# Performance work log

Hardware: AMD Instinct MI355X
Metric: run time of the kernel (lower is better)

The kernel has to match this reference:

```python
import jax, jax.numpy as jnp
import numpy as np
import math

B, S, DIM = 2, 2048, 4096
NH, NKV, HD = 32, 8, 128
N_REP = NH // NKV


def _rope_freqs(seq_len, head_dim, theta=10000.0):
    inv = 1.0 / (theta ** (np.arange(0, head_dim, 2)[: head_dim // 2].astype(np.float32) / head_dim))
    ang = np.outer(np.arange(seq_len, dtype=np.float32), inv)  # [S, HD/2]
    return jnp.asarray(np.cos(ang)), jnp.asarray(np.sin(ang))


def apply_rope(x, cos, sin):
    # x: [B, S, H, HD]; pairs along last dim act as complex numbers
    xr = x.reshape(*x.shape[:-1], HD // 2, 2)
    real, imag = xr[..., 0], xr[..., 1]
    c = cos[None, :, None, :]
    s = sin[None, :, None, :]
    out_r = real * c - imag * s
    out_i = real * s + imag * c
    return jnp.stack([out_r, out_i], axis=-1).reshape(x.shape)


def setup_inputs() -> dict:
    key = jax.random.key(0)
    ks = jax.random.split(key, 6)
    scale = 1.0 / math.sqrt(DIM)
    cos, sin = _rope_freqs(S, HD)
    return {
        "x": jax.random.normal(ks[0], (B, S, DIM), jnp.float32),
        "wq": jax.random.normal(ks[1], (DIM, NH * HD), jnp.float32) * scale,
        "wk": jax.random.normal(ks[2], (DIM, NKV * HD), jnp.float32) * scale,
        "wv": jax.random.normal(ks[3], (DIM, NKV * HD), jnp.float32) * scale,
        "wo": jax.random.normal(ks[4], (NH * HD, DIM), jnp.float32) * scale,
        "cache_k": jnp.zeros((B, S, NKV, HD), jnp.float32),
        "cache_v": jnp.zeros((B, S, NKV, HD), jnp.float32),
        "freqs_cos": cos,
        "freqs_sin": sin,
        "start_pos": 0,
    }


def reference(x, wq, wk, wv, wo, cache_k, cache_v, freqs_cos, freqs_sin, start_pos):
    b, s, _ = x.shape
    xq = (x @ wq).reshape(b, s, NH, HD)
    xk = (x @ wk).reshape(b, s, NKV, HD)
    xv = (x @ wv).reshape(b, s, NKV, HD)

    xq = apply_rope(xq, freqs_cos, freqs_sin)
    xk = apply_rope(xk, freqs_cos, freqs_sin)

    # KV-cache write
    cache_k = jax.lax.dynamic_update_slice(cache_k, xk, (0, start_pos, 0, 0))
    cache_v = jax.lax.dynamic_update_slice(cache_v, xv, (0, start_pos, 0, 0))
    keys = cache_k[:b, : start_pos + s]    # [B, T, NKV, HD]
    values = cache_v[:b, : start_pos + s]

    # GQA repeat_kv: each kv head repeated n_rep times consecutively
    keys = jnp.repeat(keys, N_REP, axis=2)      # [B, T, NH, HD]
    values = jnp.repeat(values, N_REP, axis=2)

    scores = jnp.einsum("bqhd,bkhd->bhqk", xq, keys) / math.sqrt(HD)
    probs = jax.nn.softmax(scores.astype(jnp.float32), axis=-1).astype(xq.dtype)
    out = jnp.einsum("bhqk,bkhd->bqhd", probs, values)
    out = out.reshape(b, s, NH * HD)
    return out @ wo
```

## Files before the change

### kernel.cpp

```cpp
#include <hip/hip_runtime.h>

#define S_LEN 2048
#define DIMC  4096
#define NH    32
#define NKV   8
#define HD    128
#define BATCH 2
#define M_TOT (BATCH*S_LEN)
#define N_QKV (DIMC + 2*NKV*HD)

typedef unsigned short u16;
typedef unsigned int   uint32;
typedef __attribute__((ext_vector_type(8))) short  short8;
typedef __attribute__((ext_vector_type(4))) float  f32x4;
typedef __attribute__((ext_vector_type(4))) float  fvec4;
typedef __attribute__((ext_vector_type(4))) unsigned short u16x4;

__device__ __forceinline__ u16 f2bf(float f) {
    union { float f; unsigned u; } v; v.f = f;
    unsigned r = v.u + 0x7FFFu + ((v.u >> 16) & 1u);
    return (u16)(r >> 16);
}
__device__ __forceinline__ float bf2f(u16 h) {
    union { unsigned u; float f; } v; v.u = ((unsigned)h) << 16;
    return v.f;
}

__device__ __forceinline__ void gload_lds16(const void* g, void* l) {
    __builtin_amdgcn_global_load_lds(
        (const __attribute__((address_space(1))) void*)g,
        (__attribute__((address_space(3))) void*)l, 16, 0, 0);
}

__global__ void cvt_f32_bf16(const float* __restrict__ in, u16* __restrict__ out, int n4) {
    int i = blockIdx.x * 256 + threadIdx.x;
    if (i >= n4) return;
    fvec4 v = ((const fvec4*)in)[i];
    u16x4 o;
    o[0] = f2bf(v[0]); o[1] = f2bf(v[1]); o[2] = f2bf(v[2]); o[3] = f2bf(v[3]);
    ((u16x4*)out)[i] = o;
}

__global__ void transpose_cvt(const float* __restrict__ in, u16* __restrict__ out,
                              int K, int N) {
    __shared__ float tile[32][33];
    int k0 = blockIdx.y * 32, n0 = blockIdx.x * 32;
    int t = threadIdx.x;
    int r = t >> 3, c4 = (t & 7) * 4;
    fvec4 v = *(const fvec4*)&in[(size_t)(k0 + r) * N + n0 + c4];
    tile[r][c4 + 0] = v[0]; tile[r][c4 + 1] = v[1];
    tile[r][c4 + 2] = v[2]; tile[r][c4 + 3] = v[3];
    __syncthreads();
    u16x4 o;
    o[0] = f2bf(tile[c4 + 0][r]); o[1] = f2bf(tile[c4 + 1][r]);
    o[2] = f2bf(tile[c4 + 2][r]); o[3] = f2bf(tile[c4 + 3][r]);
    *(u16x4*)&out[(size_t)(n0 + r) * K + k0 + c4] = o;
}

#define FEN asm volatile("" ::: "memory")
#define BAR1 do { FEN; __builtin_amdgcn_s_barrier(); \
                  asm volatile("s_waitcnt lgkmcnt(0)" ::: "memory"); } while(0)
#define BAR2 do { FEN; __builtin_amdgcn_s_barrier(); FEN; } while(0)

#define LDA(bufc, mh) do { _Pragma("unroll") for (int q_=0;q_<4;++q_) \
    _Pragma("unroll") for (int ks_=0;ks_<2;++ks_) \
    a[q_][ks_] = *(const short8*)(lds + ((bufc)*65536 + ((mh)*4+q_)*2048 + ks_*1024) + aB); } while(0)

#define LDB(bs, bufc, nh) do { _Pragma("unroll") for (int p_=0;p_<2;++p_) \
    _Pragma("unroll") for (int ks_=0;ks_<2;++ks_) \
    bs[p_][ks_] = *(const short8*)(lds + ((bufc)*65536 + ((nh)*2+p_)*2048 + ks_*1024) + bB); } while(0)

#define MM(mh, nh, bs) do { __builtin_amdgcn_s_setprio(1); \
  _Pragma("unroll") for (int ks_=0;ks_<2;++ks_) \
  _Pragma("unroll") for (int q_=0;q_<4;++q_) \
  _Pragma("unroll") for (int p_=0;p_<2;++p_) \
    acc[(mh)*4+q_][(nh)*2+p_] = __builtin_amdgcn_mfma_f32_16x16x32_bf16( \
        a[q_][ks_], bs[p_][ks_], acc[(mh)*4+q_][(nh)*2+p_], 0, 0, 0); \
  __builtin_amdgcn_s_setprio(0); } while(0)

#define STG(mat, half, bufS, t) do { \
    const char* gp_ = (mat) ? (const char*)Bt : (const char*)A; \
    const uint32* go_ = (mat) ? goB[half] : goA[half]; \
    gload_lds16(gp_ + (size_t)go_[0] + (size_t)(t)*128, \
                lds + ((bufS)*65536 + (mat)*32768 + (half)*16384) + s0*1024); \
    gload_lds16(gp_ + (size_t)go_[1] + (size_t)(t)*128, \
                lds + ((bufS)*65536 + (mat)*32768 + (half)*16384) + s1*1024); \
} while(0)

template<int EPI>
__global__ __launch_bounds__(512, 2) void gemm256(
    const u16* __restrict__ A, const u16* __restrict__ Bt,
    u16* __restrict__ q_raw, u16* __restrict__ k_raw, u16* __restrict__ v_t,
    float* __restrict__ outf, int Kdim)
{
    __shared__ __align__(16) char lds[131072];
    const int t = threadIdx.x, lane = t & 63, w = t >> 6;
    const int wm = w >> 2, wn = w & 3;
    const int c16 = lane & 15, g = lane >> 4;
    const int m0 = blockIdx.y * 256, n0 = blockIdx.x * 256;
    const int K2 = Kdim * 2;
    const int NT = Kdim >> 6, NITER = NT >> 1;

    const int lanebyte = c16 * 64 + ((g * 16) ^ ((c16 & 8) << 2));
    const int aB = wm * 16384 + lanebyte;
    const int bB = 32768 + (wn >> 1) * 16384 + (wn & 1) * 8192 + lanebyte;

    const int s0 = w, s1 = w + 8;
    const int stg_swz = ((lane & 3) * 16) ^ ((lane >> 5) << 5);
    uint32 goA[2][2], goB[2][2];
    #pragma unroll
    for (int h = 0; h < 2; ++h)
        #pragma unroll
        for (int ii = 0; ii < 2; ++ii) {
            int s = w + ii * 8;
            int rr = h * 128 + (s >> 1) * 16 + (lane >> 2);
            int kb = (s & 1) * 64 + stg_swz;
            goA[h][ii] = (uint32)(m0 + rr) * K2 + kb;
            goB[h][ii] = (uint32)(n0 + rr) * K2 + kb;
        }

    f32x4 acc[8][4] = {};
    short8 a[4][2], b0[2][2], b1[2][2];

    STG(1, 0, 0, 0); STG(0, 0, 0, 0); STG(1, 1, 0, 0); STG(0, 1, 0, 0);
    STG(1, 0, 1, 1); STG(0, 0, 1, 1);
    asm volatile("s_waitcnt vmcnt(4)" ::: "memory");
    BAR2;

    for (int it = 0; it < NITER; ++it) {
        const int T1 = 2 * it + 1;
        const int TN = 2 * it + 2;
        const bool nl = (it < NITER - 1);
        LDA(0, 0); LDB(b0, 0, 0);
        STG(1, 1, 1, T1);
        BAR1; MM(0, 0, b0); BAR2;
        LDB(b1, 0, 1);
        STG(0, 1, 1, T1);
        BAR1; MM(0, 1, b1); BAR2;
        LDA(0, 1);
        if (nl) STG(1, 0, 0, TN);
        BAR1; MM(1, 1, b1); BAR2;
        if (nl) { STG(0, 0, 0, TN);
                  asm volatile("s_waitcnt vmcnt(4)" ::: "memory"); }
        else    { asm volatile("s_waitcnt vmcnt(0)" ::: "memory"); }
        BAR1; MM(1, 0, b0); BAR2;
        LDA(1, 0); LDB(b0, 1, 0);
        if (nl) STG(1, 1, 0, TN);
        BAR1; MM(0, 0, b0); BAR2;
        LDB(b1, 1, 1);
        if (nl) STG(0, 1, 0, TN);
        BAR1; MM(0, 1, b1); BAR2;
        LDA(1, 1);
        if (nl) STG(1, 0, 1, TN + 1);
        BAR1; MM(1, 1, b1); BAR2;
        if (nl) STG(0, 0, 1, TN + 1);
        asm volatile("s_waitcnt vmcnt(4)" ::: "memory");
        BAR1; MM(1, 0, b0); BAR2;
    }

    #pragma unroll
    for (int fm = 0; fm < 8; ++fm) {
        int mbase = m0 + wm * 128 + fm * 16 + g * 4;
        #pragma unroll
        for (int fn = 0; fn < 4; ++fn) {
            int n = n0 + wn * 64 + fn * 16 + c16;
            #pragma unroll
            for (int r = 0; r < 4; ++r) {
                int m = mbase + r;
                float val = acc[fm][fn][r];
                if (EPI == 0) {
                    int bb = m >> 11, s = m & (S_LEN - 1);
                    u16 bv = f2bf(val);
                    if (n < DIMC) {
                        int h = n >> 7, d = n & 127;
                        q_raw[(((size_t)bb * NH + h) * S_LEN + s) * HD + d] = bv;
                    } else if (n < DIMC + NKV * HD) {
                        int h = (n - DIMC) >> 7, d = n & 127;
                        k_raw[(((size_t)bb * NKV + h) * S_LEN + s) * HD + d] = bv;
                    } else {
                        int h = (n - DIMC - NKV * HD) >> 7, d = n & 127;
                        v_t[(((size_t)bb * NKV + h) * HD + d) * S_LEN + s] = bv;
                    }
                } else {
                    outf[(size_t)m * DIMC + n] = val;
                }
            }
        }
    }
}

__global__ void rope_kernel(u16* __restrict__ q, u16* __restrict__ k,
                            const float* __restrict__ cosr, const float* __restrict__ sinr) {
    const int NQ = BATCH * NH * S_LEN * 16;
    const int NK = BATCH * NKV * S_LEN * 16;
    int idx = blockIdx.x * 256 + threadIdx.x;
    u16* ptr; int s; float scale; int ci;
    if (idx < NQ) {
        int row = idx >> 4; s = row & (S_LEN - 1);
        ptr = q + (size_t)idx * 8; scale = 0.08838834764831845f; ci = idx & 15;
    } else if (idx < NQ + NK) {
        int i2 = idx - NQ; int row = i2 >> 4; s = row & (S_LEN - 1);
        ptr = k + (size_t)i2 * 8; scale = 1.0f; ci = i2 & 15;
    } else return;
    int p0 = ci * 4;
    fvec4 c  = *(const fvec4*)&cosr[s * 64 + p0];
    fvec4 sn = *(const fvec4*)&sinr[s * 64 + p0];
    short8 v = *(const short8*)ptr;
    short8 o;
    #pragma unroll
    for (int p = 0; p < 4; ++p) {
        float re = bf2f((u16)v[2 * p]), im = bf2f((u16)v[2 * p + 1]);
        o[2 * p]     = (short)f2bf((re * c[p] - im * sn[p]) * scale);
        o[2 * p + 1] = (short)f2bf((re * sn[p] + im * c[p]) * scale);
    }
    *(short8*)ptr = o;
}

#define KVB 64
__global__ __launch_bounds__(256, 2) void attn_kernel(
    const u16* __restrict__ q_r, const u16* __restrict__ k_r,
    const u16* __restrict__ v_t, u16* __restrict__ att)
{
    __shared__ u16 kT[2][KVB * HD];
    __shared__ u16 vT[2][HD * KVB];
    __shared__ u16 pT[4][32 * KVB];
    int qt = blockIdx.x, h = blockIdx.y, b = blockIdx.z;
    int hkv = h >> 2;
    int t = threadIdx.x, lane = t & 63, w = t >> 6;
    int g = lane >> 4, c16 = lane & 15;

    const u16* Q = q_r + (((size_t)b * NH + h) * S_LEN + qt * 128 + w * 32) * HD;
    const u16* K = k_r + ((size_t)b * NKV + hkv) * S_LEN * HD;
    const u16* V = v_t + ((size_t)b * NKV + hkv) * HD * S_LEN;
    u16* pl = pT[w];

    short8 qf[2][4];
    #pragma unroll
    for (int rt = 0; rt < 2; ++rt)
        #pragma unroll
        for (int ks = 0; ks < 4; ++ks)
            qf[rt][ks] = *(const short8*)&Q[(rt * 16 + c16) * HD + ks * 32 + g * 8];

    float m_run[2][4], l_run[2][4];
    #pragma unroll
    for (int rt = 0; rt < 2; ++rt)
        #pragma unroll
        for (int j = 0; j < 4; ++j) { m_run[rt][j] = -1e30f; l_run[rt][j] = 0.f; }
    f32x4 acc_o[2][8] = {};

    #pragma unroll
    for (int i = 0; i < 4; ++i) {
        int cb = i * 256 + w * 64, c = cb + lane;
        { int row = c >> 4, lb = (c & 15) * 16, gb = lb ^ ((row & 7) << 4);
          gload_lds16(&K[(size_t)row * HD + (gb >> 1)], &kT[0][cb * 8]); }
        { int row = c >> 3, lb = (c & 7) * 16, gb = lb ^ ((row & 7) << 4);
          gload_lds16(&V[(size_t)row * S_LEN + (gb >> 1)], &vT[0][cb * 8]); }
    }
    __syncthreads();

    int buf = 0;
    for (int tt = 0; tt < S_LEN / KVB; ++tt) {
        if (tt < S_LEN / KVB - 1) {
            int kv0 = (tt + 1) * KVB;
            #pragma unroll
            for (int i = 0; i < 4; ++i) {
                int cb = i * 256 + w * 64, c = cb + lane;
                { int row = c >> 4, lb = (c & 15) * 16, gb = lb ^ ((row & 7) << 4);
                  gload_lds16(&K[(size_t)(kv0 + row) * HD + (gb >> 1)], &kT[buf ^ 1][cb * 8]); }
                { int row = c >> 3, lb = (c & 7) * 16, gb = lb ^ ((row & 7) << 4);
                  gload_lds16(&V[(size_t)row * S_LEN + kv0 + (gb >> 1)], &vT[buf ^ 1][cb * 8]); }
            }
        }
        const u16* kb = kT[buf];
        const u16* vb = vT[buf];

        f32x4 accs[2][4] = {};
        #pragma unroll
        for (int ks = 0; ks < 4; ++ks) {
            int lb = ks * 64 + g * 16;
            #pragma unroll
            for (int ct = 0; ct < 4; ++ct) {
                int r = ct * 16 + c16;
                short8 kf = *(const short8*)((const char*)kb + r * 256 + (lb ^ ((r & 7) << 4)));
                accs[0][ct] = __builtin_amdgcn_mfma_f32_16x16x32_bf16(qf[0][ks], kf, accs[0][ct], 0, 0, 0);
                accs[1][ct] = __builtin_amdgcn_mfma_f32_16x16x32_bf16(qf[1][ks], kf, accs[1][ct], 0, 0, 0);
            }
        }

        float alpha[2][4];
        #pragma unroll
        for (int rt = 0; rt < 2; ++rt)
            #pragma unroll
            for (int j = 0; j < 4; ++j) {
                float mx = fmaxf(fmaxf(accs[rt][0][j], accs[rt][1][j]),
                                 fmaxf(accs[rt][2][j], accs[rt][3][j]));
                mx = fmaxf(mx, __shfl_xor(mx, 1, 64));
                mx = fmaxf(mx, __shfl_xor(mx, 2, 64));
                mx = fmaxf(mx, __shfl_xor(mx, 4, 64));
                mx = fmaxf(mx, __shfl_xor(mx, 8, 64));
                float mn = fmaxf(m_run[rt][j], mx);
                alpha[rt][j] = __expf(m_run[rt][j] - mn);
                m_run[rt][j] = mn;
            }
        #pragma unroll
        for (int rt = 0; rt < 2; ++rt)
            #pragma unroll
            for (int j = 0; j < 4; ++j) {
                int row = rt * 16 + g * 4 + j;
                float ps = 0.f;
                #pragma unroll
                for (int ct = 0; ct < 4; ++ct) {
                    float p = __expf(accs[rt][ct][j] - m_run[rt][j]);
                    ps += p;
                    int boff = row * 128 + (((ct * 16 + c16) * 2) ^ ((row & 7) << 4));
                    *(u16*)((char*)pl + boff) = f2bf(p);
                }
                l_run[rt][j] = l_run[rt][j] * alpha[rt][j] + ps;
            }
        #pragma unroll
        for (int rt = 0; rt < 2; ++rt)
            #pragma unroll
            for (int dt = 0; dt < 8; ++dt)
                #pragma unroll
                for (int j = 0; j < 4; ++j) acc_o[rt][dt][j] *= alpha[rt][j];

        #pragma unroll
        for (int ks2 = 0; ks2 < 2; ++ks2) {
            int lb = ks2 * 64 + g * 16;
            short8 pf[2];
            #pragma unroll
            for (int rt = 0; rt < 2; ++rt) {
                int row = rt * 16 + c16;
                pf[rt] = *(const short8*)((const char*)pl + row * 128 + (lb ^ ((row & 7) << 4)));
            }
            #pragma unroll
            for (int dt = 0; dt < 8; ++dt) {
                int r = dt * 16 + c16;
                short8 vf = *(const short8*)((const char*)vb + r * 128 + (lb ^ ((r & 7) << 4)));
                acc_o[0][dt] = __builtin_amdgcn_mfma_f32_16x16x32_bf16(pf[0], vf, acc_o[0][dt], 0, 0, 0);
                acc_o[1][dt] = __builtin_amdgcn_mfma_f32_16x16x32_bf16(pf[1], vf, acc_o[1][dt], 0, 0, 0);
            }
        }
        __syncthreads();
        buf ^= 1;
    }

    #pragma unroll
    for (int rt = 0; rt < 2; ++rt)
        #pragma unroll
        for (int j = 0; j < 4; ++j) {
            float l = l_run[rt][j];
            l += __shfl_xor(l, 1, 64);
            l += __shfl_xor(l, 2, 64);
            l += __shfl_xor(l, 4, 64);
            l += __shfl_xor(l, 8, 64);
            float rl = 1.f / l;
            size_t mrow = (size_t)b * S_LEN + qt * 128 + w * 32 + rt * 16 + g * 4 + j;
            #pragma unroll
            for (int dt = 0; dt < 8; ++dt)
                att[mrow * DIMC + h * HD + dt * 16 + c16] = f2bf(acc_o[rt][dt][j] * rl);
        }
}

extern "C" void kernel_launch(void* const* d_in, const int* in_sizes, int n_in,
                              void* d_out, int out_size, void* d_ws, size_t ws_size,
                              hipStream_t stream) {
    const float* x    = (const float*)d_in[0];
    const float* wq   = (const float*)d_in[1];
    const float* wk   = (const float*)d_in[2];
    const float* wv   = (const float*)d_in[3];
    const float* wo   = (const float*)d_in[4];
    const float* cosr = (const float*)d_in[7];
    const float* sinr = (const float*)d_in[8];
    float* out = (float*)d_out;

    char* ws = (char*)d_ws;
    u16* x_bf   = (u16*)(ws);
    u16* wqkv_t = (u16*)(ws + 33554432);
    u16* wo_t   = (u16*)(ws + 83886080);
    u16* q_r    = (u16*)(ws + 117440512);
    u16* k_r    = (u16*)(ws + 150994944);
    u16* v_t    = (u16*)(ws + 159383552);
    u16* att    = (u16*)(ws + 167772160);

    cvt_f32_bf16<<<16384, 256, 0, stream>>>(x, x_bf, (M_TOT * DIMC) / 4);
    transpose_cvt<<<dim3(128, 128), 256, 0, stream>>>(wq, wqkv_t, DIMC, 4096);
    transpose_cvt<<<dim3(32, 128), 256, 0, stream>>>(wk, wqkv_t + (size_t)4096 * DIMC, DIMC, 1024);
    transpose_cvt<<<dim3(32, 128), 256, 0, stream>>>(wv, wqkv_t + (size_t)5120 * DIMC, DIMC, 1024);
    transpose_cvt<<<dim3(128, 128), 256, 0, stream>>>(wo, wo_t, 4096, DIMC);

    gemm256<0><<<dim3(N_QKV / 256, M_TOT / 256), 512, 0, stream>>>(
        x_bf, wqkv_t, q_r, k_r, v_t, nullptr, DIMC);

    rope_kernel<<<(BATCH * (NH + NKV) * S_LEN * 16) / 256, 256, 0, stream>>>(q_r, k_r, cosr, sinr);

    attn_kernel<<<dim3(S_LEN / 128, NH, BATCH), 256, 0, stream>>>(q_r, k_r, v_t, att);

    gemm256<1><<<dim3(DIMC / 256, M_TOT / 256), 512, 0, stream>>>(
        att, wo_t, nullptr, nullptr, nullptr, out, DIMC);
}
```

Baseline: 867.1 us.

## Rewrite attention with 32x32 MFMA, register-resident P, lazy rescale; swizzle GEMM grid

The attention kernel is rebuilt around 32x32x16 bf16 MFMAs computing S^T, so each lane holds a query column. Probabilities are packed with cvt_pk_bf16 and permlane32 swaps straight into MFMA operands, which removes the LDS round trip for P. Softmax now uses exp2 with log2e folded into the Q scale, and the output is rescaled only when the running max grows past a threshold. Blocks grow to 512 threads covering 256 queries. The GEMM also remaps workgroup IDs across 8 groups (likely for XCD/L2 locality). The risks are exact-softmax accuracy under the lazy max threshold and higher register pressure.

```diff
diff --git a/kernel.cpp b/kernel.cpp
--- a/kernel.cpp
+++ b/kernel.cpp
@@ -11,10 +11,11 @@
 
 typedef unsigned short u16;
 typedef unsigned int   uint32;
-typedef __attribute__((ext_vector_type(8))) short  short8;
-typedef __attribute__((ext_vector_type(4))) float  f32x4;
-typedef __attribute__((ext_vector_type(4))) float  fvec4;
-typedef __attribute__((ext_vector_type(4))) unsigned short u16x4;
+typedef __attribute__((ext_vector_type(8)))  short short8;
+typedef __attribute__((ext_vector_type(4)))  float f32x4;
+typedef __attribute__((ext_vector_type(16))) float f32x16;
+typedef __attribute__((ext_vector_type(4)))  float fvec4;
+typedef __attribute__((ext_vector_type(4)))  unsigned short u16x4;
 
 __device__ __forceinline__ u16 f2bf(float f) {
     union { float f; unsigned u; } v; v.f = f;
@@ -24,6 +25,17 @@
 __device__ __forceinline__ float bf2f(u16 h) {
     union { unsigned u; float f; } v; v.u = ((unsigned)h) << 16;
     return v.f;
+}
+__device__ __forceinline__ float exp2_fast(float x) {
+    return __builtin_amdgcn_exp2f(x);
+}
+__device__ __forceinline__ unsigned cvtpk_bf16(float lo, float hi) {
+    unsigned r;
+    asm volatile("v_cvt_pk_bf16_f32 %0, %1, %2" : "=v"(r) : "v"(lo), "v"(hi));
+    return r;
+}
+__device__ __forceinline__ void pl32swap(unsigned &a, unsigned &b) {
+    asm volatile("v_permlane32_swap_b32 %0, %1" : "+v"(a), "+v"(b));
 }
 
 __device__ __forceinline__ void gload_lds16(const void* g, void* l) {
@@ -97,9 +109,15 @@
     const int t = threadIdx.x, lane = t & 63, w = t >> 6;
     const int wm = w >> 2, wn = w & 3;
     const int c16 = lane & 15, g = lane >> 4;
-    const int m0 = blockIdx.y * 256, n0 = blockIdx.x * 256;
+
+    const int nwgx = gridDim.x, nwg = nwgx * gridDim.y;
+    int orig = blockIdx.y * nwgx + blockIdx.x;
+    int cpx = nwg >> 3;
+    int wg = (orig & 7) * cpx + (orig >> 3);
+    const int m0 = (wg / nwgx) * 256, n0 = (wg % nwgx) * 256;
+
     const int K2 = Kdim * 2;
-    const int NT = Kdim >> 6, NITER = NT >> 1;
+    const int NITER = Kdim >> 7;
 
     const int lanebyte = c16 * 64 + ((g * 16) ^ ((c16 & 8) << 2));
     const int aB = wm * 16384 + lanebyte;
@@ -197,7 +215,7 @@
     u16* ptr; int s; float scale; int ci;
     if (idx < NQ) {
         int row = idx >> 4; s = row & (S_LEN - 1);
-        ptr = q + (size_t)idx * 8; scale = 0.08838834764831845f; ci = idx & 15;
+        ptr = q + (size_t)idx * 8; scale = 0.12751744f; ci = idx & 15;
     } else if (idx < NQ + NK) {
         int i2 = idx - NQ; int row = i2 >> 4; s = row & (S_LEN - 1);
         ptr = k + (size_t)i2 * 8; scale = 1.0f; ci = i2 & 15;
@@ -217,149 +235,141 @@
 }
 
 #define KVB 64
-__global__ __launch_bounds__(256, 2) void attn_kernel(
+#define THR2 11.0f
+
+#define STAGE_KV(DB, KV0) do { \
+    _Pragma("unroll") for (int i_ = 0; i_ < 2; ++i_) { \
+        int c_ = w * 2 + i_; \
+        int kr_ = c_ * 4 + (lane >> 4); \
+        int kb_ = ((lane & 15) * 16) ^ ((kr_ & 7) << 4); \
+        gload_lds16(&K[(size_t)((KV0) + kr_) * HD + (kb_ >> 1)], &kT[DB][c_ * 512]); \
+        int vr_ = c_ * 8 + (lane >> 3); \
+        int vb_ = ((lane & 7) * 16) ^ ((vr_ & 7) << 4); \
+        gload_lds16(&V[(size_t)vr_ * S_LEN + (KV0) + (vb_ >> 1)], &vT[DB][c_ * 512]); \
+    } } while(0)
+
+#define PKSLOT(SREG, KS, KOFF) do { \
+    float p0 = exp2_fast(SREG[(KOFF)+0] - m2), p1 = exp2_fast(SREG[(KOFF)+1] - m2); \
+    float p2 = exp2_fast(SREG[(KOFF)+2] - m2), p3 = exp2_fast(SREG[(KOFF)+3] - m2); \
+    float p4 = exp2_fast(SREG[(KOFF)+4] - m2), p5 = exp2_fast(SREG[(KOFF)+5] - m2); \
+    float p6 = exp2_fast(SREG[(KOFF)+6] - m2), p7 = exp2_fast(SREG[(KOFF)+7] - m2); \
+    psum += (p0+p1)+(p2+p3)+((p4+p5)+(p6+p7)); \
+    unsigned a01 = cvtpk_bf16(p0,p1), a23 = cvtpk_bf16(p2,p3); \
+    unsigned b01 = cvtpk_bf16(p4,p5), b23 = cvtpk_bf16(p6,p7); \
+    pl32swap(a01, b01); pl32swap(a23, b23); \
+    union { short8 s8; unsigned u[4]; } pu; \
+    pu.u[0] = a01; pu.u[1] = a23; pu.u[2] = b01; pu.u[3] = b23; \
+    const int vcb_ = ((KS)*32 + hi*16) ^ ((l31 & 7) << 4); \
+    _Pragma("unroll") for (int dt_ = 0; dt_ < 4; ++dt_) { \
+        short8 vb = *(const short8*)((const char*)vbuf + (dt_*32 + l31)*128 + vcb_); \
+        o_acc[dt_] = __builtin_amdgcn_mfma_f32_32x32x16_bf16(pu.s8, vb, o_acc[dt_], 0, 0, 0); \
+    } } while(0)
+
+__global__ __launch_bounds__(512, 2) void attn32(
     const u16* __restrict__ q_r, const u16* __restrict__ k_r,
     const u16* __restrict__ v_t, u16* __restrict__ att)
 {
     __shared__ u16 kT[2][KVB * HD];
     __shared__ u16 vT[2][HD * KVB];
-    __shared__ u16 pT[4][32 * KVB];
-    int qt = blockIdx.x, h = blockIdx.y, b = blockIdx.z;
-    int hkv = h >> 2;
-    int t = threadIdx.x, lane = t & 63, w = t >> 6;
-    int g = lane >> 4, c16 = lane & 15;
-
-    const u16* Q = q_r + (((size_t)b * NH + h) * S_LEN + qt * 128 + w * 32) * HD;
+    __shared__ float aT[8][32];
+    const int qt = blockIdx.x, h = blockIdx.y, b = blockIdx.z;
+    const int hkv = h >> 2;
+    const int t = threadIdx.x, lane = t & 63, w = t >> 6;
+    const int l31 = lane & 31, hi = lane >> 5;
+
+    const u16* Q = q_r + (((size_t)b * NH + h) * S_LEN + qt * 256 + w * 32 + l31) * HD;
     const u16* K = k_r + ((size_t)b * NKV + hkv) * S_LEN * HD;
     const u16* V = v_t + ((size_t)b * NKV + hkv) * HD * S_LEN;
-    u16* pl = pT[w];
-
-    short8 qf[2][4];
+
+    short8 qb[8];
     #pragma unroll
-    for (int rt = 0; rt < 2; ++rt)
-        #pragma unroll
-        for (int ks = 0; ks < 4; ++ks)
-            qf[rt][ks] = *(const short8*)&Q[(rt * 16 + c16) * HD + ks * 32 + g * 8];
-
-    float m_run[2][4], l_run[2][4];
-    #pragma unroll
-    for (int rt = 0; rt < 2; ++rt)
-        #pragma unroll
-        for (int j = 0; j < 4; ++j) { m_run[rt][j] = -1e30f; l_run[rt][j] = 0.f; }
-    f32x4 acc_o[2][8] = {};
-
-    #pragma unroll
-    for (int i = 0; i < 4; ++i) {
-        int cb = i * 256 + w * 64, c = cb + lane;
-        { int row = c >> 4, lb = (c & 15) * 16, gb = lb ^ ((row & 7) << 4);
-          gload_lds16(&K[(size_t)row * HD + (gb >> 1)], &kT[0][cb * 8]); }
-        { int row = c >> 3, lb = (c & 7) * 16, gb = lb ^ ((row & 7) << 4);
-          gload_lds16(&V[(size_t)row * S_LEN + (gb >> 1)], &vT[0][cb * 8]); }
-    }
+    for (int ks = 0; ks < 8; ++ks)
+        qb[ks] = *(const short8*)&Q[ks * 16 + hi * 8];
+
+    float m2 = -3e38f, l_run = 0.f;
+    f32x16 o_acc[4] = {};
+
+    STAGE_KV(0, 0);
     __syncthreads();
 
     int buf = 0;
     for (int tt = 0; tt < S_LEN / KVB; ++tt) {
-        if (tt < S_LEN / KVB - 1) {
-            int kv0 = (tt + 1) * KVB;
+        if (tt < S_LEN / KVB - 1) STAGE_KV(buf ^ 1, (tt + 1) * KVB);
+        const u16* kbuf = kT[buf];
+        const u16* vbuf = vT[buf];
+
+        f32x16 sA = {}, sB = {};
+        #pragma unroll
+        for (int ks = 0; ks < 8; ++ks) {
+            int cb = (ks * 32 + hi * 16) ^ ((l31 & 7) << 4);
+            short8 ka0 = *(const short8*)((const char*)kbuf + l31 * 256 + cb);
+            short8 ka1 = *(const short8*)((const char*)kbuf + (32 + l31) * 256 + cb);
+            sA = __builtin_amdgcn_mfma_f32_32x32x16_bf16(ka0, qb[ks], sA, 0, 0, 0);
+            sB = __builtin_amdgcn_mfma_f32_32x32x16_bf16(ka1, qb[ks], sB, 0, 0, 0);
+        }
+
+        float mx = sA[0];
+        #pragma unroll
+        for (int e = 1; e < 16; ++e) mx = fmaxf(mx, sA[e]);
+        #pragma unroll
+        for (int e = 0; e < 16; ++e) mx = fmaxf(mx, sB[e]);
+        mx = fmaxf(mx, __shfl_xor(mx, 32));
+
+        if (__any(mx > m2 + THR2)) {
+            float mnew = fmaxf(m2, mx);
+            float al = exp2_fast(m2 - mnew);
+            m2 = mnew;
+            l_run *= al;
+            if (hi == 0) aT[w][l31] = al;
+            asm volatile("s_waitcnt lgkmcnt(0)" ::: "memory");
+            __builtin_amdgcn_sched_barrier(0);
+            f32x4 av0 = *(f32x4*)&aT[w][hi * 4];
+            f32x4 av1 = *(f32x4*)&aT[w][8 + hi * 4];
+            f32x4 av2 = *(f32x4*)&aT[w][16 + hi * 4];
+            f32x4 av3 = *(f32x4*)&aT[w][24 + hi * 4];
             #pragma unroll
-            for (int i = 0; i < 4; ++i) {
-                int cb = i * 256 + w * 64, c = cb + lane;
-                { int row = c >> 4, lb = (c & 15) * 16, gb = lb ^ ((row & 7) << 4);
-                  gload_lds16(&K[(size_t)(kv0 + row) * HD + (gb >> 1)], &kT[buf ^ 1][cb * 8]); }
-                { int row = c >> 3, lb = (c & 7) * 16, gb = lb ^ ((row & 7) << 4);
-                  gload_lds16(&V[(size_t)row * S_LEN + kv0 + (gb >> 1)], &vT[buf ^ 1][cb * 8]); }
-            }
+            for (int dt = 0; dt < 4; ++dt)
+                #pragma unroll
+                for (int e = 0; e < 4; ++e) {
+                    o_acc[dt][e]      *= av0[e];
+                    o_acc[dt][4 + e]  *= av1[e];
+                    o_acc[dt][8 + e]  *= av2[e];
+                    o_acc[dt][12 + e] *= av3[e];
+                }
         }
-        const u16* kb = kT[buf];
-        const u16* vb = vT[buf];
-
-        f32x4 accs[2][4] = {};
-        #pragma unroll
-        for (int ks = 0; ks < 4; ++ks) {
-            int lb = ks * 64 + g * 16;
-            #pragma unroll
-            for (int ct = 0; ct < 4; ++ct) {
-                int r = ct * 16 + c16;
-                short8 kf = *(const short8*)((const char*)kb + r * 256 + (lb ^ ((r & 7) << 4)));
-                accs[0][ct] = __builtin_amdgcn_mfma_f32_16x16x32_bf16(qf[0][ks], kf, accs[0][ct], 0, 0, 0);
-                accs[1][ct] = __builtin_amdgcn_mfma_f32_16x16x32_bf16(qf[1][ks], kf, accs[1][ct], 0, 0, 0);
-            }
-        }
-
-        float alpha[2][4];
-        #pragma unroll
-        for (int rt = 0; rt < 2; ++rt)
-            #pragma unroll
-            for (int j = 0; j < 4; ++j) {
-                float mx = fmaxf(fmaxf(accs[rt][0][j], accs[rt][1][j]),
-                                 fmaxf(accs[rt][2][j], accs[rt][3][j]));
-                mx = fmaxf(mx, __shfl_xor(mx, 1, 64));
-                mx = fmaxf(mx, __shfl_xor(mx, 2, 64));
-                mx = fmaxf(mx, __shfl_xor(mx, 4, 64));
-                mx = fmaxf(mx, __shfl_xor(mx, 8, 64));
-                float mn = fmaxf(m_run[rt][j], mx);
-                alpha[rt][j] = __expf(m_run[rt][j] - mn);
-                m_run[rt][j] = mn;
-            }
-        #pragma unroll
-        for (int rt = 0; rt < 2; ++rt)
-            #pragma unroll
-            for (int j = 0; j < 4; ++j) {
-                int row = rt * 16 + g * 4 + j;
-                float ps = 0.f;
-                #pragma unroll
-                for (int ct = 0; ct < 4; ++ct) {
-                    float p = __expf(accs[rt][ct][j] - m_run[rt][j]);
-                    ps += p;
-                    int boff = row * 128 + (((ct * 16 + c16) * 2) ^ ((row & 7) << 4));
-                    *(u16*)((char*)pl + boff) = f2bf(p);
-                }
-                l_run[rt][j] = l_run[rt][j] * alpha[rt][j] + ps;
-            }
-        #pragma unroll
-        for (int rt = 0; rt < 2; ++rt)
-            #pragma unroll
-            for (int dt = 0; dt < 8; ++dt)
-                #pragma unroll
-                for (int j = 0; j < 4; ++j) acc_o[rt][dt][j] *= alpha[rt][j];
-
-        #pragma unroll
-        for (int ks2 = 0; ks2 < 2; ++ks2) {
-            int lb = ks2 * 64 + g * 16;
-            short8 pf[2];
-            #pragma unroll
-            for (int rt = 0; rt < 2; ++rt) {
-                int row = rt * 16 + c16;
-                pf[rt] = *(const short8*)((const char*)pl + row * 128 + (lb ^ ((row & 7) << 4)));
-            }
-            #pragma unroll
-            for (int dt = 0; dt < 8; ++dt) {
-                int r = dt * 16 + c16;
-                short8 vf = *(const short8*)((const char*)vb + r * 128 + (lb ^ ((r & 7) << 4)));
-                acc_o[0][dt] = __builtin_amdgcn_mfma_f32_16x16x32_bf16(pf[0], vf, acc_o[0][dt], 0, 0, 0);
-                acc_o[1][dt] = __builtin_amdgcn_mfma_f32_16x16x32_bf16(pf[1], vf, acc_o[1][dt], 0, 0, 0);
-            }
-        }
+
+        float psum = 0.f;
+        PKSLOT(sA, 0, 0);
+        PKSLOT(sA, 1, 8);
+        PKSLOT(sB, 2, 0);
+        PKSLOT(sB, 3, 8);
+        l_run += psum;
+
         __syncthreads();
         buf ^= 1;
     }
 
+    float l_tot = l_run + __shfl_xor(l_run, 32);
+    float rl = 1.f / l_tot;
+    if (hi == 0) aT[w][l31] = rl;
+    asm volatile("s_waitcnt lgkmcnt(0)" ::: "memory");
+    __builtin_amdgcn_sched_barrier(0);
+    f32x4 rv0 = *(f32x4*)&aT[w][hi * 4];
+    f32x4 rv1 = *(f32x4*)&aT[w][8 + hi * 4];
+    f32x4 rv2 = *(f32x4*)&aT[w][16 + hi * 4];
+    f32x4 rv3 = *(f32x4*)&aT[w][24 + hi * 4];
+    const size_t mbase = (size_t)b * S_LEN + qt * 256 + w * 32;
     #pragma unroll
-    for (int rt = 0; rt < 2; ++rt)
-        #pragma unroll
-        for (int j = 0; j < 4; ++j) {
-            float l = l_run[rt][j];
-            l += __shfl_xor(l, 1, 64);
-            l += __shfl_xor(l, 2, 64);
-            l += __shfl_xor(l, 4, 64);
-            l += __shfl_xor(l, 8, 64);
-            float rl = 1.f / l;
-            size_t mrow = (size_t)b * S_LEN + qt * 128 + w * 32 + rt * 16 + g * 4 + j;
-            #pragma unroll
-            for (int dt = 0; dt < 8; ++dt)
-                att[mrow * DIMC + h * HD + dt * 16 + c16] = f2bf(acc_o[rt][dt][j] * rl);
+    for (int dt = 0; dt < 4; ++dt) {
+        int dcol = h * HD + dt * 32 + l31;
+        #pragma unroll
+        for (int e = 0; e < 4; ++e) {
+            att[(mbase + 8 * 0 + 4 * hi + e) * DIMC + dcol] = f2bf(o_acc[dt][e]      * rv0[e]);
+            att[(mbase + 8 * 1 + 4 * hi + e) * DIMC + dcol] = f2bf(o_acc[dt][4 + e]  * rv1[e]);
+            att[(mbase + 8 * 2 + 4 * hi + e) * DIMC + dcol] = f2bf(o_acc[dt][8 + e]  * rv2[e]);
+            att[(mbase + 8 * 3 + 4 * hi + e) * DIMC + dcol] = f2bf(o_acc[dt][12 + e] * rv3[e]);
         }
+    }
 }
 
 extern "C" void kernel_launch(void* const* d_in, const int* in_sizes, int n_in,
@@ -394,7 +404,7 @@
 
     rope_kernel<<<(BATCH * (NH + NKV) * S_LEN * 16) / 256, 256, 0, stream>>>(q_r, k_r, cosr, sinr);
 
-    attn_kernel<<<dim3(S_LEN / 128, NH, BATCH), 256, 0, stream>>>(q_r, k_r, v_t, att);
+    attn32<<<dim3(S_LEN / 256, NH, BATCH), 512, 0, stream>>>(q_r, k_r, v_t, att);
 
     gemm256<1><<<dim3(DIMC / 256, M_TOT / 256), 512, 0, stream>>>(
         att, wo_t, nullptr, nullptr, nullptr, out, DIMC);
```

Measured after the change: 781.8 us. -9.8%, faster.
